# Performance work log

Measured on AMD Instinct MI355X. Metric: run time of the kernel, lower is better.

## Reference

```python
import jax, jax.numpy as jnp
import numpy as np

QUERY_DIM = 1024
KEY_DIM = 1024
NUM_HEADS = 16
HEAD_DIM = QUERY_DIM // NUM_HEADS


def setup_inputs() -> dict:
    key = jax.random.key(0)
    ks = jax.random.split(key, 12)
    B, Sq, Sk = 2, 1024, 4096

    def xavier(k, fan_in, fan_out):
        limit = np.sqrt(6.0 / (fan_in + fan_out))
        return jax.random.uniform(k, (fan_in, fan_out), jnp.float32, -limit, limit)

    return {
        "query": jax.random.normal(ks[0], (B, Sq, QUERY_DIM), jnp.float32),
        "key": jax.random.normal(ks[1], (B, Sk, KEY_DIM), jnp.float32),
        "value": jax.random.normal(ks[2], (B, Sk, KEY_DIM), jnp.float32),
        "key_mask": jax.random.randint(ks[3], (B, Sk), 0, 2, jnp.int32),
        # projection weights stored as [in, out] for x @ W
        "Wq": xavier(ks[4], QUERY_DIM, NUM_HEADS * HEAD_DIM),
        "bq": jnp.zeros((NUM_HEADS * HEAD_DIM,), jnp.float32),
        "Wk": xavier(ks[5], KEY_DIM, NUM_HEADS * HEAD_DIM),
        "bk": jnp.zeros((NUM_HEADS * HEAD_DIM,), jnp.float32),
        "Wv": xavier(ks[6], KEY_DIM, NUM_HEADS * HEAD_DIM),
        "bv": jnp.zeros((NUM_HEADS * HEAD_DIM,), jnp.float32),
        "Wo": xavier(ks[7], NUM_HEADS * HEAD_DIM, QUERY_DIM),
        "bo": jnp.zeros((QUERY_DIM,), jnp.float32),
    }


def reference(query, key, value, key_mask, Wq, bq, Wk, bk, Wv, bv, Wo, bo):
    B, Sq, _ = query.shape
    Sk = key.shape[1]
    H, D = NUM_HEADS, HEAD_DIM
    scale = 1.0 / np.sqrt(D)

    q = (query @ Wq + bq).reshape(B, Sq, H, D)   # [B,Sq,H,D]
    k = (key @ Wk + bk).reshape(B, Sk, H, D)     # [B,Sk,H,D]
    v = (value @ Wv + bv).reshape(B, Sk, H, D)

    # scores: [B,H,Sq,Sk]
    scores = jnp.einsum("bqhd,bkhd->bhqk", q, k) * scale
    mask = (key_mask == 0)[:, None, None, :]  # [B,1,1,Sk]
    scores = jnp.where(mask, jnp.float32(-1e9), scores)
    probs = jax.nn.softmax(scores, axis=-1)
    # dropout is identity at eval (p effectively 0)
    ctx = jnp.einsum("bhqk,bkhd->bqhd", probs, v).reshape(B, Sq, H * D)
    return ctx @ Wo + bo
```

## Files before the change

kernel.cpp:

```cpp
#include <hip/hip_runtime.h>
#include <stdint.h>

#define NH 16
#define HD 64
#define SQ 1024
#define SK 4096
#define DM 1024
#define MQ 2048
#define MK 8192
#define MTOT 18432

typedef short s16x8 __attribute__((ext_vector_type(8)));
typedef float f32x4 __attribute__((ext_vector_type(4)));

#define GLOAD_LDS16(g, l) __builtin_amdgcn_global_load_lds( \
    (const __attribute__((address_space(1))) void*)(g), \
    (__attribute__((address_space(3))) void*)(l), 16, 0, 0)

__device__ __forceinline__ short f2bf(float f) {
  union { float f; uint32_t u; } v; v.f = f;
  uint32_t r = (v.u + 0x7FFFu + ((v.u >> 16) & 1u)) >> 16;
  return (short)(uint16_t)r;
}
__device__ __forceinline__ short f2bf_rz(float f) {
  union { float f; uint32_t u; } v; v.f = f;
  return (short)(uint16_t)(v.u >> 16);
}

__global__ void cvt_kernel(const float* __restrict__ src, short* __restrict__ dst, int n8) {
  int stride = gridDim.x * blockDim.x;
  for (int i = blockIdx.x * blockDim.x + threadIdx.x; i < n8; i += stride) {
    const float4* s4 = (const float4*)src + 2 * (size_t)i;
    float4 a = s4[0], b = s4[1];
    s16x8 o;
    o[0] = f2bf(a.x); o[1] = f2bf(a.y); o[2] = f2bf(a.z); o[3] = f2bf(a.w);
    o[4] = f2bf(b.x); o[5] = f2bf(b.y); o[6] = f2bf(b.z); o[7] = f2bf(b.w);
    *((s16x8*)dst + i) = o;
  }
}

__global__ void twkernel(const float* __restrict__ W, short* __restrict__ Wt) {
  __shared__ __align__(16) short t[64][65];
  int lx = threadIdx.x & 63, ly = threadIdx.x >> 6;
  int c0 = (blockIdx.x & 15) * 64, r0 = (blockIdx.x >> 4) * 64;
  #pragma unroll
  for (int i = ly; i < 64; i += 4) t[i][lx] = f2bf(W[(size_t)(r0 + i) * DM + c0 + lx]);
  __syncthreads();
  #pragma unroll
  for (int i = ly; i < 64; i += 4) Wt[(size_t)(c0 + i) * DM + r0 + lx] = t[lx][i];
}

__global__ __launch_bounds__(256) void proj_gemm(
    const short* __restrict__ Acat,
    const short* __restrict__ Wqt, const short* __restrict__ Wkt, const short* __restrict__ Wvt,
    const float* __restrict__ bq, const float* __restrict__ bk, const float* __restrict__ bv,
    short* __restrict__ Qp, short* __restrict__ Kp, short* __restrict__ Vp)
{
  __shared__ __align__(16) short As[128 * 32];
  __shared__ __align__(16) short Bs[128 * 32];
  int tid = threadIdx.x, lane = tid & 63, wid = tid >> 6;
  int bm = blockIdx.x >> 3, bn = blockIdx.x & 7;
  int m0 = bm * 128, n0 = bn * 128;
  int seg = (m0 < MQ) ? 0 : (m0 < MQ + MK) ? 1 : 2;
  const short* Wt = (seg == 0) ? Wqt : (seg == 1) ? Wkt : Wvt;
  const float* bias = (seg == 0) ? bq : (seg == 1) ? bk : bv;

  int off = tid * 16;
  int arow = off >> 6;
  int acol = (off & 63) >> 1;
  int wr = wid >> 1, wc = wid & 1;
  int l15 = lane & 15, g = lane >> 4, lh8 = g * 8;

  f32x4 acc[4][4] = {};

  const short* gA0 = Acat + (size_t)(m0 + arow) * DM + acol;
  const short* gA1 = Acat + (size_t)(m0 + arow + 64) * DM + acol;
  const short* gB0 = Wt + (size_t)(n0 + arow) * DM + acol;
  const short* gB1 = Wt + (size_t)(n0 + arow + 64) * DM + acol;

  for (int kt = 0; kt < 32; ++kt) {
    int k0 = kt * 32;
    __syncthreads();
    GLOAD_LDS16(gA0 + k0, (char*)As + off);
    GLOAD_LDS16(gA1 + k0, (char*)As + off + 4096);
    GLOAD_LDS16(gB0 + k0, (char*)Bs + off);
    GLOAD_LDS16(gB1 + k0, (char*)Bs + off + 4096);
    __syncthreads();
    s16x8 af[4], bfr[4];
    #pragma unroll
    for (int mi = 0; mi < 4; ++mi)
      af[mi] = *(const s16x8*)((const char*)As + ((wr * 64 + mi * 16 + l15) * 32 + lh8) * 2);
    #pragma unroll
    for (int ni = 0; ni < 4; ++ni)
      bfr[ni] = *(const s16x8*)((const char*)Bs + ((wc * 64 + ni * 16 + l15) * 32 + lh8) * 2);
    #pragma unroll
    for (int mi = 0; mi < 4; ++mi)
      #pragma unroll
      for (int ni = 0; ni < 4; ++ni)
        acc[mi][ni] = __builtin_amdgcn_mfma_f32_16x16x32_bf16(af[mi], bfr[ni], acc[mi][ni], 0, 0, 0);
  }

  __syncthreads();

  if (seg == 2) {
    short* tw = (short*)As + wid * 288;
    int vbase = m0 - (MQ + MK) + wr * 64;
    #pragma unroll
    for (int mi = 0; mi < 4; ++mi) {
      int vr = vbase + mi * 16 + l15;
      int bb2 = vr >> 12, sk = vr & 4095;
      #pragma unroll
      for (int ni = 0; ni < 4; ++ni) {
        int col = n0 + wc * 64 + ni * 16;
        int h = col >> 6, d0 = col & 63;
        float bb = bias[col + l15];
        #pragma unroll
        for (int r = 0; r < 4; ++r)
          tw[(g * 4 + r) * 18 + l15] = f2bf(acc[mi][ni][r] + bb);
        #pragma unroll
        for (int j = 0; j < 4; ++j) {
          int dl = g * 4 + j;
          Vp[((size_t)(bb2 * NH + h) * HD + d0 + dl) * SK + sk] = tw[l15 * 18 + dl];
        }
      }
    }
  } else {
    char* tw2 = (char*)As + wid * 2048;
    int hh = (n0 + wc * 64) >> 6;
    short* outp = (seg == 0) ? Qp : Kp;
    int sdim = (seg == 0) ? SQ : SK;
    int rbase = (seg == 0) ? m0 : m0 - MQ;
    int rmask = (seg == 0) ? 1023 : 4095;
    int rshift = (seg == 0) ? 10 : 12;
    #pragma unroll
    for (int mi = 0; mi < 4; ++mi) {
      #pragma unroll
      for (int ni = 0; ni < 4; ++ni) {
        float bb = bias[n0 + wc * 64 + ni * 16 + l15];
        #pragma unroll
        for (int r = 0; r < 4; ++r) {
          int rw = g * 4 + r;
          *(short*)(tw2 + rw * 128 + (((ni * 16 + l15) * 2) ^ ((rw & 7) << 4))) =
              f2bf(acc[mi][ni][r] + bb);
        }
      }
      asm volatile("s_waitcnt lgkmcnt(0)" ::: "memory");
      #pragma unroll
      for (int pp = 0; pp < 2; ++pp) {
        int lr = pp * 8 + (lane >> 3);
        int ce = (lane & 7) * 8;
        s16x8 v8 = *(const s16x8*)(tw2 + lr * 128 + ((ce * 2) ^ ((lr & 7) << 4)));
        int row = rbase + wr * 64 + mi * 16 + lr;
        int bI = row >> rshift, s = row & rmask;
        *(s16x8*)(outp + ((size_t)(bI * NH + hh) * sdim + s) * HD + ce) = v8;
      }
      asm volatile("s_waitcnt lgkmcnt(0)" ::: "memory");
    }
  }
}

__global__ __launch_bounds__(256) void attn_kernel(
    const short* __restrict__ Qp, const short* __restrict__ Kp, const short* __restrict__ Vp,
    const int* __restrict__ kmask, short* __restrict__ ctx)
{
  __shared__ __align__(16) short Ks[2][64 * 64];
  __shared__ __align__(16) short Vs[2][64 * 64];
  __shared__ __align__(16) short Ps[4][16 * 64];
  __shared__ float madd[SK];

  int tid = threadIdx.x, lane = tid & 63, wid = tid >> 6;
  int bh = blockIdx.x & 31, qt = blockIdx.x >> 5;
  int b = bh >> 4, h = bh & 15;
  const short* Qb = Qp + (size_t)bh * SQ * HD;
  const short* Kb = Kp + (size_t)bh * SK * HD;
  const short* Vb = Vp + (size_t)bh * HD * SK;
  const int* kmb = kmask + b * SK;

  for (int i = tid; i < SK; i += 256) madd[i] = kmb[i] ? -8.0f : -1e9f;

  int l15 = lane & 15, g = lane >> 4, lh8 = g * 8;
  int q0 = qt * 64 + wid * 16;
  int swz = (l15 & 7) << 4;

  s16x8 aq[2];
  aq[0] = *(const s16x8*)(Qb + (size_t)(q0 + l15) * HD + lh8);
  aq[1] = *(const s16x8*)(Qb + (size_t)(q0 + l15) * HD + 32 + lh8);

  s16x8 ones;
  #pragma unroll
  for (int j = 0; j < 8; ++j) ones[j] = (short)0x3F80;

  f32x4 o[4] = {};
  f32x4 ol = {};

  int srow = tid >> 3, scEl = (tid & 7) * 8;
  int wsoff = srow * 128 + ((scEl * 2) ^ ((srow & 7) << 4));

  s16x8 rk0, rk1, rv0, rv1;
#define ALOADS(t) { \
    rk0 = *(const s16x8*)(Kb + (size_t)((t) * 64 + srow) * HD + scEl); \
    rk1 = *(const s16x8*)(Kb + (size_t)((t) * 64 + srow + 32) * HD + scEl); \
    rv0 = *(const s16x8*)(Vb + (size_t)srow * SK + (t) * 64 + scEl); \
    rv1 = *(const s16x8*)(Vb + (size_t)(srow + 32) * SK + (t) * 64 + scEl); }
#define STAGE(bi) { \
    char* kb_ = (char*)Ks[bi]; char* vb_ = (char*)Vs[bi]; \
    *(s16x8*)(kb_ + wsoff) = rk0; *(s16x8*)(kb_ + wsoff + 4096) = rk1; \
    *(s16x8*)(vb_ + wsoff) = rv0; *(s16x8*)(vb_ + wsoff + 4096) = rv1; }

  ALOADS(0); STAGE(0); ALOADS(1);
  __syncthreads();

  const float sscale = 0.18033688f;
  for (int t = 0; t < 64; ++t) {
    int cur = t & 1;
    if (t < 63) STAGE(cur ^ 1);
    if (t < 62) ALOADS(t + 2);
    const char* KsB = (const char*)Ks[cur];
    const char* VsB = (const char*)Vs[cur];

    f32x4 sc[4] = {};
    __builtin_amdgcn_s_setprio(1);
    #pragma unroll
    for (int ni = 0; ni < 4; ++ni) {
      #pragma unroll
      for (int ks = 0; ks < 2; ++ks) {
        s16x8 kf = *(const s16x8*)(KsB + (ni * 16 + l15) * 128 + ((ks * 64 + g * 16) ^ swz));
        sc[ni] = __builtin_amdgcn_mfma_f32_16x16x32_bf16(aq[ks], kf, sc[ni], 0, 0, 0);
      }
    }
    __builtin_amdgcn_s_setprio(0);

    char* PsW = (char*)&Ps[wid][0];
    #pragma unroll
    for (int ni = 0; ni < 4; ++ni) {
      float ma = madd[t * 64 + ni * 16 + l15];
      #pragma unroll
      for (int r = 0; r < 4; ++r) {
        float p = exp2f(sc[ni][r] * sscale + ma);
        int prow = g * 4 + r;
        *(short*)(PsW + prow * 128 + (((ni * 16 + l15) * 2) ^ ((prow & 7) << 4))) = f2bf_rz(p);
      }
    }
    asm volatile("s_waitcnt lgkmcnt(0)" ::: "memory");

    __builtin_amdgcn_s_setprio(1);
    #pragma unroll
    for (int ks2 = 0; ks2 < 2; ++ks2) {
      s16x8 pa = *(const s16x8*)(PsW + l15 * 128 + ((ks2 * 64 + g * 16) ^ swz));
      #pragma unroll
      for (int nd = 0; nd < 4; ++nd) {
        s16x8 vf = *(const s16x8*)(VsB + (nd * 16 + l15) * 128 + ((ks2 * 64 + g * 16) ^ swz));
        o[nd] = __builtin_amdgcn_mfma_f32_16x16x32_bf16(pa, vf, o[nd], 0, 0, 0);
      }
      ol = __builtin_amdgcn_mfma_f32_16x16x32_bf16(pa, ones, ol, 0, 0, 0);
    }
    __builtin_amdgcn_s_setprio(0);
    __syncthreads();
  }
#undef ALOADS
#undef STAGE

  #pragma unroll
  for (int nd = 0; nd < 4; ++nd) {
    #pragma unroll
    for (int r = 0; r < 4; ++r) {
      int q = q0 + g * 4 + r;
      int d = nd * 16 + l15;
      float val = o[nd][r] / ol[r];
      ctx[((size_t)(b * SQ + q)) * DM + h * HD + d] = f2bf(val);
    }
  }
}

__global__ __launch_bounds__(256) void out_gemm(
    const short* __restrict__ Actx, const short* __restrict__ Wot,
    const float* __restrict__ bo, float* __restrict__ out)
{
  __shared__ __align__(16) short As[128 * 32];
  __shared__ __align__(16) short Bs[128 * 32];
  int tid = threadIdx.x, lane = tid & 63, wid = tid >> 6;
  int bm = blockIdx.x >> 3, bn = blockIdx.x & 7;
  int m0 = bm * 128, n0 = bn * 128;

  int off = tid * 16;
  int arow = off >> 6;
  int acol = (off & 63) >> 1;
  int wr = wid >> 1, wc = wid & 1;
  int l15 = lane & 15, lh8 = (lane >> 4) * 8;

  f32x4 acc[4][4] = {};

  const short* gA0 = Actx + (size_t)(m0 + arow) * DM + acol;
  const short* gA1 = Actx + (size_t)(m0 + arow + 64) * DM + acol;
  const short* gB0 = Wot + (size_t)(n0 + arow) * DM + acol;
  const short* gB1 = Wot + (size_t)(n0 + arow + 64) * DM + acol;

  for (int kt = 0; kt < 32; ++kt) {
    int k0 = kt * 32;
    __syncthreads();
    GLOAD_LDS16(gA0 + k0, (char*)As + off);
    GLOAD_LDS16(gA1 + k0, (char*)As + off + 4096);
    GLOAD_LDS16(gB0 + k0, (char*)Bs + off);
    GLOAD_LDS16(gB1 + k0, (char*)Bs + off + 4096);
    __syncthreads();
    s16x8 af[4], bfr[4];
    #pragma unroll
    for (int mi = 0; mi < 4; ++mi)
      af[mi] = *(const s16x8*)((const char*)As + ((wr * 64 + mi * 16 + l15) * 32 + lh8) * 2);
    #pragma unroll
    for (int ni = 0; ni < 4; ++ni)
      bfr[ni] = *(const s16x8*)((const char*)Bs + ((wc * 64 + ni * 16 + l15) * 32 + lh8) * 2);
    #pragma unroll
    for (int mi = 0; mi < 4; ++mi)
      #pragma unroll
      for (int ni = 0; ni < 4; ++ni)
        acc[mi][ni] = __builtin_amdgcn_mfma_f32_16x16x32_bf16(af[mi], bfr[ni], acc[mi][ni], 0, 0, 0);
  }

  #pragma unroll
  for (int mi = 0; mi < 4; ++mi) {
    #pragma unroll
    for (int ni = 0; ni < 4; ++ni) {
      int col = n0 + wc * 64 + ni * 16 + l15;
      float bb = bo[col];
      #pragma unroll
      for (int r = 0; r < 4; ++r) {
        int row = m0 + wr * 64 + mi * 16 + (lane >> 4) * 4 + r;
        out[(size_t)row * DM + col] = acc[mi][ni][r] + bb;
      }
    }
  }
}

extern "C" void kernel_launch(void* const* d_in, const int* in_sizes, int n_in,
                              void* d_out, int out_size, void* d_ws, size_t ws_size,
                              hipStream_t stream) {
  const float* query = (const float*)d_in[0];
  const float* key   = (const float*)d_in[1];
  const float* value = (const float*)d_in[2];
  const int*   kmask = (const int*)d_in[3];
  const float* Wq = (const float*)d_in[4];
  const float* bq = (const float*)d_in[5];
  const float* Wk = (const float*)d_in[6];
  const float* bk = (const float*)d_in[7];
  const float* Wv = (const float*)d_in[8];
  const float* bv = (const float*)d_in[9];
  const float* Wo = (const float*)d_in[10];
  const float* bo = (const float*)d_in[11];
  float* out = (float*)d_out;

  char* ws = (char*)d_ws;
  short* Acat = (short*)ws;
  short* Wqt  = (short*)(ws + (size_t)37748736);
  short* Wkt  = Wqt + 1048576;
  short* Wvt  = Wkt + 1048576;
  short* Wot  = Wvt + 1048576;
  short* Qp   = Wot + 1048576;
  short* Kp   = Qp + 2097152;
  short* Vp   = Kp + 8388608;
  short* ctx  = Vp + 8388608;

  short* qbf = Acat;
  short* kbf = Acat + 2097152;
  short* vbf = Acat + 2097152 + 8388608;

  cvt_kernel<<<1024, 256, 0, stream>>>(query, qbf, 2097152 / 8);
  cvt_kernel<<<2048, 256, 0, stream>>>(key,   kbf, 8388608 / 8);
  cvt_kernel<<<2048, 256, 0, stream>>>(value, vbf, 8388608 / 8);
  twkernel<<<256, 256, 0, stream>>>(Wq, Wqt);
  twkernel<<<256, 256, 0, stream>>>(Wk, Wkt);
  twkernel<<<256, 256, 0, stream>>>(Wv, Wvt);
  twkernel<<<256, 256, 0, stream>>>(Wo, Wot);
  proj_gemm<<<1152, 256, 0, stream>>>(Acat, Wqt, Wkt, Wvt, bq, bk, bv, Qp, Kp, Vp);
  attn_kernel<<<512, 256, 0, stream>>>(Qp, Kp, Vp, kmask, ctx);
  out_gemm<<<128, 256, 0, stream>>>(ctx, Wot, bo, out);
}
```

Before: 341.1 us.

## Split attention over key halves with combine pass; deepen GEMM K-tiles

Measured after the change: 357.2 us. +4.7%, slower.

```diff
diff --git a/kernel.cpp b/kernel.cpp
--- a/kernel.cpp
+++ b/kernel.cpp
@@ -11,6 +11,7 @@
 #define MTOT 18432
 
 typedef short s16x8 __attribute__((ext_vector_type(8)));
+typedef short s16x4 __attribute__((ext_vector_type(4)));
 typedef float f32x4 __attribute__((ext_vector_type(4)));
 
 #define GLOAD_LDS16(g, l) __builtin_amdgcn_global_load_lds( \
@@ -39,6 +40,11 @@
   }
 }
 
+__global__ void maskf_kernel(const int* __restrict__ km, float* __restrict__ madd_g) {
+  int i = blockIdx.x * 256 + threadIdx.x;
+  if (i < 2 * SK) madd_g[i] = km[i] ? -8.0f : -1e9f;
+}
+
 __global__ void twkernel(const float* __restrict__ W, short* __restrict__ Wt) {
   __shared__ __align__(16) short t[64][65];
   int lx = threadIdx.x & 63, ly = threadIdx.x >> 6;
@@ -56,8 +62,8 @@
     const float* __restrict__ bq, const float* __restrict__ bk, const float* __restrict__ bv,
     short* __restrict__ Qp, short* __restrict__ Kp, short* __restrict__ Vp)
 {
-  __shared__ __align__(16) short As[128 * 32];
-  __shared__ __align__(16) short Bs[128 * 32];
+  __shared__ __align__(16) short As[128 * 64];
+  __shared__ __align__(16) short Bs[128 * 64];
   int tid = threadIdx.x, lane = tid & 63, wid = tid >> 6;
   int bm = blockIdx.x >> 3, bn = blockIdx.x & 7;
   int m0 = bm * 128, n0 = bn * 128;
@@ -65,39 +71,45 @@
   const short* Wt = (seg == 0) ? Wqt : (seg == 1) ? Wkt : Wvt;
   const float* bias = (seg == 0) ? bq : (seg == 1) ? bk : bv;
 
-  int off = tid * 16;
-  int arow = off >> 6;
-  int acol = (off & 63) >> 1;
+  int rs = tid >> 3;
+  int cb8 = (tid & 7) * 8;
   int wr = wid >> 1, wc = wid & 1;
-  int l15 = lane & 15, g = lane >> 4, lh8 = g * 8;
+  int l15 = lane & 15, g = lane >> 4;
 
   f32x4 acc[4][4] = {};
 
-  const short* gA0 = Acat + (size_t)(m0 + arow) * DM + acol;
-  const short* gA1 = Acat + (size_t)(m0 + arow + 64) * DM + acol;
-  const short* gB0 = Wt + (size_t)(n0 + arow) * DM + acol;
-  const short* gB1 = Wt + (size_t)(n0 + arow + 64) * DM + acol;
-
-  for (int kt = 0; kt < 32; ++kt) {
-    int k0 = kt * 32;
+  const short* gA = Acat + (size_t)(m0 + rs) * DM + cb8;
+  const short* gB = Wt + (size_t)(n0 + rs) * DM + cb8;
+  char* lA = (char*)As + tid * 16;
+  char* lB = (char*)Bs + tid * 16;
+
+  for (int kt = 0; kt < 16; ++kt) {
+    int k0 = kt * 64;
     __syncthreads();
-    GLOAD_LDS16(gA0 + k0, (char*)As + off);
-    GLOAD_LDS16(gA1 + k0, (char*)As + off + 4096);
-    GLOAD_LDS16(gB0 + k0, (char*)Bs + off);
-    GLOAD_LDS16(gB1 + k0, (char*)Bs + off + 4096);
+    GLOAD_LDS16(gA + k0,            lA);
+    GLOAD_LDS16(gA + 32 * DM + k0,  lA + 4096);
+    GLOAD_LDS16(gA + 64 * DM + k0,  lA + 8192);
+    GLOAD_LDS16(gA + 96 * DM + k0,  lA + 12288);
+    GLOAD_LDS16(gB + k0,            lB);
+    GLOAD_LDS16(gB + 32 * DM + k0,  lB + 4096);
+    GLOAD_LDS16(gB + 64 * DM + k0,  lB + 8192);
+    GLOAD_LDS16(gB + 96 * DM + k0,  lB + 12288);
     __syncthreads();
-    s16x8 af[4], bfr[4];
-    #pragma unroll
-    for (int mi = 0; mi < 4; ++mi)
-      af[mi] = *(const s16x8*)((const char*)As + ((wr * 64 + mi * 16 + l15) * 32 + lh8) * 2);
-    #pragma unroll
-    for (int ni = 0; ni < 4; ++ni)
-      bfr[ni] = *(const s16x8*)((const char*)Bs + ((wc * 64 + ni * 16 + l15) * 32 + lh8) * 2);
-    #pragma unroll
-    for (int mi = 0; mi < 4; ++mi)
+    #pragma unroll
+    for (int kk = 0; kk < 2; ++kk) {
+      s16x8 af[4], bfr[4];
+      #pragma unroll
+      for (int mi = 0; mi < 4; ++mi)
+        af[mi] = *(const s16x8*)((const char*)As + (wr * 64 + mi * 16 + l15) * 128 + kk * 64 + g * 16);
       #pragma unroll
       for (int ni = 0; ni < 4; ++ni)
-        acc[mi][ni] = __builtin_amdgcn_mfma_f32_16x16x32_bf16(af[mi], bfr[ni], acc[mi][ni], 0, 0, 0);
+        bfr[ni] = *(const s16x8*)((const char*)Bs + (wc * 64 + ni * 16 + l15) * 128 + kk * 64 + g * 16);
+      #pragma unroll
+      for (int mi = 0; mi < 4; ++mi)
+        #pragma unroll
+        for (int ni = 0; ni < 4; ++ni)
+          acc[mi][ni] = __builtin_amdgcn_mfma_f32_16x16x32_bf16(af[mi], bfr[ni], acc[mi][ni], 0, 0, 0);
+    }
   }
 
   __syncthreads();
@@ -161,22 +173,20 @@
 
 __global__ __launch_bounds__(256) void attn_kernel(
     const short* __restrict__ Qp, const short* __restrict__ Kp, const short* __restrict__ Vp,
-    const int* __restrict__ kmask, short* __restrict__ ctx)
+    const float* __restrict__ madd_g, float* __restrict__ po, float* __restrict__ pl)
 {
   __shared__ __align__(16) short Ks[2][64 * 64];
   __shared__ __align__(16) short Vs[2][64 * 64];
   __shared__ __align__(16) short Ps[4][16 * 64];
-  __shared__ float madd[SK];
 
   int tid = threadIdx.x, lane = tid & 63, wid = tid >> 6;
-  int bh = blockIdx.x & 31, qt = blockIdx.x >> 5;
-  int b = bh >> 4, h = bh & 15;
+  int sub = blockIdx.x & 63, qt = blockIdx.x >> 6;
+  int bh = sub >> 1, half = sub & 1;
+  int b = bh >> 4;
   const short* Qb = Qp + (size_t)bh * SQ * HD;
-  const short* Kb = Kp + (size_t)bh * SK * HD;
-  const short* Vb = Vp + (size_t)bh * HD * SK;
-  const int* kmb = kmask + b * SK;
-
-  for (int i = tid; i < SK; i += 256) madd[i] = kmb[i] ? -8.0f : -1e9f;
+  const short* Kb = Kp + (size_t)bh * SK * HD + (size_t)half * 2048 * HD;
+  const short* Vb = Vp + (size_t)bh * HD * SK + half * 2048;
+  const float* mab = madd_g + b * SK + half * 2048;
 
   int l15 = lane & 15, g = lane >> 4, lh8 = g * 8;
   int q0 = qt * 64 + wid * 16;
@@ -211,10 +221,10 @@
   __syncthreads();
 
   const float sscale = 0.18033688f;
-  for (int t = 0; t < 64; ++t) {
+  for (int t = 0; t < 32; ++t) {
     int cur = t & 1;
-    if (t < 63) STAGE(cur ^ 1);
-    if (t < 62) ALOADS(t + 2);
+    if (t < 31) STAGE(cur ^ 1);
+    if (t < 30) ALOADS(t + 2);
     const char* KsB = (const char*)Ks[cur];
     const char* VsB = (const char*)Vs[cur];
 
@@ -233,7 +243,7 @@
     char* PsW = (char*)&Ps[wid][0];
     #pragma unroll
     for (int ni = 0; ni < 4; ++ni) {
-      float ma = madd[t * 64 + ni * 16 + l15];
+      float ma = mab[t * 64 + ni * 16 + l15];
       #pragma unroll
       for (int r = 0; r < 4; ++r) {
         float p = exp2f(sc[ni][r] * sscale + ma);
@@ -260,61 +270,92 @@
 #undef ALOADS
 #undef STAGE
 
+  float* poB = po + (size_t)blockIdx.x * 4096;
   #pragma unroll
   for (int nd = 0; nd < 4; ++nd) {
     #pragma unroll
     for (int r = 0; r < 4; ++r) {
-      int q = q0 + g * 4 + r;
-      int d = nd * 16 + l15;
-      float val = o[nd][r] / ol[r];
-      ctx[((size_t)(b * SQ + q)) * DM + h * HD + d] = f2bf(val);
-    }
-  }
+      int ql = wid * 16 + g * 4 + r;
+      poB[ql * 64 + nd * 16 + l15] = o[nd][r];
+    }
+  }
+  if (l15 == 0) {
+    #pragma unroll
+    for (int r = 0; r < 4; ++r)
+      pl[(size_t)blockIdx.x * 64 + wid * 16 + g * 4 + r] = ol[r];
+  }
+}
+
+__global__ __launch_bounds__(256) void combine_kernel(
+    const float* __restrict__ po, const float* __restrict__ pl, short* __restrict__ ctx)
+{
+  int tg = blockIdx.x * 256 + threadIdx.x;
+  int d4 = (tg & 15) * 4;
+  int idx = tg >> 4;
+  int bh = idx >> 10, qrow = idx & 1023;
+  int qt = qrow >> 6, ql = qrow & 63;
+  int pid0 = qt * 64 + bh * 2;
+  const float4 a = *(const float4*)(po + (size_t)pid0 * 4096 + ql * 64 + d4);
+  const float4 c = *(const float4*)(po + (size_t)(pid0 + 1) * 4096 + ql * 64 + d4);
+  float rl = 1.0f / (pl[(size_t)pid0 * 64 + ql] + pl[(size_t)(pid0 + 1) * 64 + ql]);
+  s16x4 outv;
+  outv[0] = f2bf((a.x + c.x) * rl);
+  outv[1] = f2bf((a.y + c.y) * rl);
+  outv[2] = f2bf((a.z + c.z) * rl);
+  outv[3] = f2bf((a.w + c.w) * rl);
+  int b = bh >> 4, h = bh & 15;
+  *(s16x4*)(ctx + ((size_t)(b * SQ + qrow)) * DM + h * HD + d4) = outv;
 }
 
 __global__ __launch_bounds__(256) void out_gemm(
     const short* __restrict__ Actx, const short* __restrict__ Wot,
     const float* __restrict__ bo, float* __restrict__ out)
 {
-  __shared__ __align__(16) short As[128 * 32];
-  __shared__ __align__(16) short Bs[128 * 32];
+  __shared__ __align__(16) short As[128 * 64];
+  __shared__ __align__(16) short Bs[128 * 64];
   int tid = threadIdx.x, lane = tid & 63, wid = tid >> 6;
   int bm = blockIdx.x >> 3, bn = blockIdx.x & 7;
   int m0 = bm * 128, n0 = bn * 128;
 
-  int off = tid * 16;
-  int arow = off >> 6;
-  int acol = (off & 63) >> 1;
+  int rs = tid >> 3;
+  int cb8 = (tid & 7) * 8;
   int wr = wid >> 1, wc = wid & 1;
-  int l15 = lane & 15, lh8 = (lane >> 4) * 8;
+  int l15 = lane & 15, g = lane >> 4;
 
   f32x4 acc[4][4] = {};
 
-  const short* gA0 = Actx + (size_t)(m0 + arow) * DM + acol;
-  const short* gA1 = Actx + (size_t)(m0 + arow + 64) * DM + acol;
-  const short* gB0 = Wot + (size_t)(n0 + arow) * DM + acol;
-  const short* gB1 = Wot + (size_t)(n0 + arow + 64) * DM + acol;
-
-  for (int kt = 0; kt < 32; ++kt) {
-    int k0 = kt * 32;
+  const short* gA = Actx + (size_t)(m0 + rs) * DM + cb8;
+  const short* gB = Wot + (size_t)(n0 + rs) * DM + cb8;
+  char* lA = (char*)As + tid * 16;
+  char* lB = (char*)Bs + tid * 16;
+
+  for (int kt = 0; kt < 16; ++kt) {
+    int k0 = kt * 64;
     __syncthreads();
-    GLOAD_LDS16(gA0 + k0, (char*)As + off);
-    GLOAD_LDS16(gA1 + k0, (char*)As + off + 4096);
-    GLOAD_LDS16(gB0 + k0, (char*)Bs + off);
-    GLOAD_LDS16(gB1 + k0, (char*)Bs + off + 4096);
+    GLOAD_LDS16(gA + k0,            lA);
+    GLOAD_LDS16(gA + 32 * DM + k0,  lA + 4096);
+    GLOAD_LDS16(gA + 64 * DM + k0,  lA + 8192);
+    GLOAD_LDS16(gA + 96 * DM + k0,  lA + 12288);
+    GLOAD_LDS16(gB + k0,            lB);
+    GLOAD_LDS16(gB + 32 * DM + k0,  lB + 4096);
+    GLOAD_LDS16(gB + 64 * DM + k0,  lB + 8192);
+    GLOAD_LDS16(gB + 96 * DM + k0,  lB + 12288);
     __syncthreads();
-    s16x8 af[4], bfr[4];
-    #pragma unroll
-    for (int mi = 0; mi < 4; ++mi)
-      af[mi] = *(const s16x8*)((const char*)As + ((wr * 64 + mi * 16 + l15) * 32 + lh8) * 2);
-    #pragma unroll
-    for (int ni = 0; ni < 4; ++ni)
-      bfr[ni] = *(const s16x8*)((const char*)Bs + ((wc * 64 + ni * 16 + l15) * 32 + lh8) * 2);
-    #pragma unroll
-    for (int mi = 0; mi < 4; ++mi)
+    #pragma unroll
+    for (int kk = 0; kk < 2; ++kk) {
+      s16x8 af[4], bfr[4];
+      #pragma unroll
+      for (int mi = 0; mi < 4; ++mi)
+        af[mi] = *(const s16x8*)((const char*)As + (wr * 64 + mi * 16 + l15) * 128 + kk * 64 + g * 16);
       #pragma unroll
       for (int ni = 0; ni < 4; ++ni)
-        acc[mi][ni] = __builtin_amdgcn_mfma_f32_16x16x32_bf16(af[mi], bfr[ni], acc[mi][ni], 0, 0, 0);
+        bfr[ni] = *(const s16x8*)((const char*)Bs + (wc * 64 + ni * 16 + l15) * 128 + kk * 64 + g * 16);
+      #pragma unroll
+      for (int mi = 0; mi < 4; ++mi)
+        #pragma unroll
+        for (int ni = 0; ni < 4; ++ni)
+          acc[mi][ni] = __builtin_amdgcn_mfma_f32_16x16x32_bf16(af[mi], bfr[ni], acc[mi][ni], 0, 0, 0);
+    }
   }
 
   #pragma unroll
@@ -325,7 +366,7 @@
       float bb = bo[col];
       #pragma unroll
       for (int r = 0; r < 4; ++r) {
-        int row = m0 + wr * 64 + mi * 16 + (lane >> 4) * 4 + r;
+        int row = m0 + wr * 64 + mi * 16 + g * 4 + r;
         out[(size_t)row * DM + col] = acc[mi][ni][r] + bb;
       }
     }
@@ -359,6 +400,10 @@
   short* Kp   = Qp + 2097152;
   short* Vp   = Kp + 8388608;
   short* ctx  = Vp + 8388608;
+  float* madd_g = (float*)(ctx + 2097152);
+
+  float* po = (float*)Acat;
+  float* pl = po + (size_t)1024 * 4096;
 
   short* qbf = Acat;
   short* kbf = Acat + 2097152;
@@ -367,11 +412,13 @@
   cvt_kernel<<<1024, 256, 0, stream>>>(query, qbf, 2097152 / 8);
   cvt_kernel<<<2048, 256, 0, stream>>>(key,   kbf, 8388608 / 8);
   cvt_kernel<<<2048, 256, 0, stream>>>(value, vbf, 8388608 / 8);
+  maskf_kernel<<<32, 256, 0, stream>>>(kmask, madd_g);
   twkernel<<<256, 256, 0, stream>>>(Wq, Wqt);
   twkernel<<<256, 256, 0, stream>>>(Wk, Wkt);
   twkernel<<<256, 256, 0, stream>>>(Wv, Wvt);
   twkernel<<<256, 256, 0, stream>>>(Wo, Wot);
   proj_gemm<<<1152, 256, 0, stream>>>(Acat, Wqt, Wkt, Wvt, bq, bk, bv, Qp, Kp, Vp);
-  attn_kernel<<<512, 256, 0, stream>>>(Qp, Kp, Vp, kmask, ctx);
+  attn_kernel<<<1024, 256, 0, stream>>>(Qp, Kp, Vp, madd_g, po, pl);
+  combine_kernel<<<2048, 256, 0, stream>>>(po, pl, ctx);
   out_gemm<<<128, 256, 0, stream>>>(ctx, Wot, bo, out);
 }
```
